# Performance work log

Measured on AMD Instinct MI355X. Metric: run time of the kernel, lower is better.

## Reference

```python
import jax, jax.numpy as jnp
import numpy as np


def _chamfer_single_directional(x, y):
    """Mean over batch of mean over points of min_j ||x_i - y_j||^2.

    x: [B, N, 3] (predicted), y: [B, M, 3] (target).
    Matches pytorch3d chamfer_distance(x, y, single_directional=True)
    with norm=2, point_reduction='mean', batch_reduction='mean'.
    """
    x2 = jnp.sum(x * x, axis=-1)                      # [B, N]
    y2 = jnp.sum(y * y, axis=-1)                      # [B, M]
    cross = jnp.einsum('bnd,bmd->bnm', x, y)          # [B, N, M]
    d2 = x2[:, :, None] + y2[:, None, :] - 2.0 * cross  # squared L2
    min_d2 = jnp.min(d2, axis=2)                      # [B, N] nearest in y
    return jnp.mean(jnp.mean(min_d2, axis=1))         # scalar


def setup_inputs() -> dict:
    key = jax.random.key(0)
    k1, k2 = jax.random.split(key)
    v = jax.random.normal(k1, (4, 8192, 3), dtype=jnp.float32)
    v_pred = jax.random.normal(k2, (4, 8192, 3), dtype=jnp.float32)
    return {"v": v, "v_pred": v_pred}


def reference(v, v_pred):
    # forward: chamfer_distance(v_pred, v, single_directional=True)
    return _chamfer_single_directional(v_pred, v)
```

## Files before the change

### kernel.cpp

```cpp
#include <hip/hip_runtime.h>

#define BB 4
#define NN 8192
#define MM 8192
#define BN (BB * NN)

#define BLK 256
#define QB  256
#define TC  1024
#define S   (MM / TC)
#define NJT (TC / 32)
#define NGRP ((NN / QB) * BB)

#define RB 32
#define GPB (NGRP / RB)

typedef __bf16 bf16x8 __attribute__((ext_vector_type(8)));
typedef float  f32x16 __attribute__((ext_vector_type(16)));


static __device__ inline void split_bf(float v, __bf16& h, __bf16& l) {
    h = (__bf16)v;
    l = (__bf16)(v - (float)h);
}

__global__ __launch_bounds__(BLK, 4) void chamfer_part(
    const float* __restrict__ y,
    const float* __restrict__ x,
    float* __restrict__ part)
{
    __shared__ uint4 FR[NJT * 64];
    __shared__ float red[QB];

    const int t   = threadIdx.x;
    const int l   = t & 63;
    const int w   = t >> 6;
    const int hi  = l >> 5;
    const int c32 = l & 31;
    const int ib  = blockIdx.x;
    const int s   = blockIdx.y;
    const int b   = blockIdx.z;
    const int g   = b * (NN / QB) + ib;

    {
        const float* xb = x + ((size_t)b * NN + (size_t)ib * QB) * 3;
        float x0 = xb[3*t+0], x1 = xb[3*t+1], x2 = xb[3*t+2];
        __bf16 h0,l0,h1,l1,h2,l2;
        split_bf(2.0f*x0, h0, l0);
        split_bf(2.0f*x1, h1, l1);
        split_bf(2.0f*x2, h2, l2);
        float nxx = -__builtin_fmaf(x2, x2, __builtin_fmaf(x1, x1, x0*x0));
        __bf16 hx, lx; split_bf(nxx, hx, lx);
        const __bf16 one = (__bf16)1.0f;
        bf16x8 g0 = {h0,h0,l0,l0,h1,h1,l1,l1};
        bf16x8 g1 = {h2,h2,l2,l2,hx,lx,one,one};
        const int at = t >> 5, col = t & 31;
        FR[at*64 +      col] = __builtin_bit_cast(uint4, g0);
        FR[at*64 + 32 + col] = __builtin_bit_cast(uint4, g1);
    }
    __syncthreads();
    const bf16x8 a0 = __builtin_bit_cast(bf16x8, FR[(w*2 + 0)*64 + l]);
    const bf16x8 a1 = __builtin_bit_cast(bf16x8, FR[(w*2 + 1)*64 + l]);
    __syncthreads();

    {
        const float* yb = y + ((size_t)b * MM + (size_t)s * TC) * 3;
        const __bf16 one = (__bf16)1.0f;
#pragma unroll
        for (int k2 = 0; k2 < 4; ++k2) {
            const int j = t + k2 * BLK;
            float y0 = yb[3*j+0], y1 = yb[3*j+1], y2 = yb[3*j+2];
            __bf16 h0,l0,h1,l1,h2,l2;
            split_bf(y0, h0, l0);
            split_bf(y1, h1, l1);
            split_bf(y2, h2, l2);
            float nyy = -__builtin_fmaf(y2, y2, __builtin_fmaf(y1, y1, y0*y0));
            __bf16 hy, ly; split_bf(nyy, hy, ly);
            bf16x8 g0 = {h0,l0,h0,l0,h1,l1,h1,l1};
            bf16x8 g1 = {h2,l2,h2,l2,one,one,hy,ly};
            const int jt = j >> 5, col = j & 31;
            FR[jt*64 +      col] = __builtin_bit_cast(uint4, g0);
            FR[jt*64 + 32 + col] = __builtin_bit_cast(uint4, g1);
        }
    }
    __syncthreads();

    f32x16 z;
#pragma unroll
    for (int r = 0; r < 16; ++r) z[r] = 0.0f;
    f32x16 best0, best1;
#pragma unroll
    for (int r = 0; r < 16; ++r) { best0[r] = -3.4e38f; best1[r] = -3.4e38f; }

#pragma unroll 1
    for (int jt = 0; jt < NJT; jt += 2) {
        const bf16x8 bf0 = __builtin_bit_cast(bf16x8, FR[jt*64 + l]);
        const bf16x8 bf1 = __builtin_bit_cast(bf16x8, FR[jt*64 + 64 + l]);
        f32x16 p = __builtin_amdgcn_mfma_f32_32x32x16_bf16(a0, bf0, z, 0, 0, 0);
        f32x16 q = __builtin_amdgcn_mfma_f32_32x32x16_bf16(a0, bf1, z, 0, 0, 0);
#pragma unroll
        for (int r = 0; r < 16; ++r)
            best0[r] = fmaxf(fmaxf(best0[r], p[r]), q[r]);
        p = __builtin_amdgcn_mfma_f32_32x32x16_bf16(a1, bf0, z, 0, 0, 0);
        q = __builtin_amdgcn_mfma_f32_32x32x16_bf16(a1, bf1, z, 0, 0, 0);
#pragma unroll
        for (int r = 0; r < 16; ++r)
            best1[r] = fmaxf(fmaxf(best1[r], p[r]), q[r]);
    }

#pragma unroll
    for (int ii = 0; ii < 2; ++ii) {
        const f32x16 bb = ii ? best1 : best0;
#pragma unroll
        for (int r = 0; r < 16; ++r) {
            float v = bb[r];
            v = fmaxf(v, __shfl_xor(v, 1, 64));
            v = fmaxf(v, __shfl_xor(v, 2, 64));
            v = fmaxf(v, __shfl_xor(v, 4, 64));
            v = fmaxf(v, __shfl_xor(v, 8, 64));
            v = fmaxf(v, __shfl_xor(v, 16, 64));
            if (c32 == 0) {
                const int qrow = (w*2 + ii)*32 + (r & 3) + 8*(r >> 2) + 4*hi;
                red[qrow] = -v;
            }
        }
    }
    __syncthreads();
    part[((size_t)g * S + s) * QB + t] = red[t];
}

__global__ __launch_bounds__(BLK) void reduce_groups(
    const float* __restrict__ part,
    float* __restrict__ ws2)
{
    const int t = threadIdx.x;
    float acc = 0.0f;
#pragma unroll
    for (int gi = 0; gi < GPB; ++gi) {
        const float* pg = part + ((size_t)(blockIdx.x * GPB + gi) * S) * QB;
        float dq = pg[t];
#pragma unroll
        for (int ss = 1; ss < S; ++ss)
            dq = fminf(dq, pg[ss * QB + t]);
        acc += dq;
    }
    for (int off = 32; off > 0; off >>= 1)
        acc += __shfl_down(acc, off, 64);
    __shared__ float wsum[4];
    if ((t & 63) == 0) wsum[t >> 6] = acc;
    __syncthreads();
    if (t == 0)
        ws2[blockIdx.x] = wsum[0] + wsum[1] + wsum[2] + wsum[3];
}

__global__ __launch_bounds__(64) void final32(
    const float* __restrict__ ws2,
    float* __restrict__ out)
{
    const int t = threadIdx.x;
    float v = (t < RB) ? ws2[t] : 0.0f;
    for (int off = 32; off > 0; off >>= 1)
        v += __shfl_down(v, off, 64);
    if (t == 0) out[0] = v * (1.0f / (float)BN);
}

extern "C" void kernel_launch(void* const* d_in, const int* in_sizes, int n_in,
                              void* d_out, int out_size, void* d_ws, size_t ws_size,
                              hipStream_t stream) {
    const float* v      = (const float*)d_in[0];
    const float* v_pred = (const float*)d_in[1];
    float* out = (float*)d_out;

    float* part = (float*)d_ws;
    float* ws2  = (float*)((char*)d_ws + (1u << 20));

    chamfer_part<<<dim3(NN / QB, S, BB), BLK, 0, stream>>>(v, v_pred, part);
    reduce_groups<<<RB, BLK, 0, stream>>>(part, ws2);
    final32<<<1, 64, 0, stream>>>(ws2, out);
}
```

Measured before the change: 73.44 us.

## Fuse chamfer over full target set with double-buffered LDS tiles, drop reduce kernel

```diff
diff --git a/kernel.cpp b/kernel.cpp
--- a/kernel.cpp
+++ b/kernel.cpp
@@ -5,15 +5,12 @@
 #define MM 8192
 #define BN (BB * NN)
 
-#define BLK 256
-#define QB  256
-#define TC  1024
-#define S   (MM / TC)
-#define NJT (TC / 32)
-#define NGRP ((NN / QB) * BB)
-
-#define RB 32
-#define GPB (NGRP / RB)
+#define QB   128
+#define BLK  512
+#define NCH  8
+#define TPC  1024
+#define NT   32
+#define NBLK ((NN / QB) * BB)
 
 typedef __bf16 bf16x8 __attribute__((ext_vector_type(8)));
 typedef float  f32x16 __attribute__((ext_vector_type(16)));
@@ -24,144 +21,154 @@
     l = (__bf16)(v - (float)h);
 }
 
-__global__ __launch_bounds__(BLK, 4) void chamfer_part(
+static __device__ inline void packB(float y0, float y1, float y2,
+                                    uint4& o0, uint4& o1) {
+    __bf16 h0,l0,h1,l1,h2,l2,hy,ly;
+    split_bf(y0, h0, l0);
+    split_bf(y1, h1, l1);
+    split_bf(y2, h2, l2);
+    float nyy = -__builtin_fmaf(y2, y2, __builtin_fmaf(y1, y1, y0*y0));
+    split_bf(nyy, hy, ly);
+    const __bf16 one = (__bf16)1.0f;
+    bf16x8 g0 = {h0,l0,h0,l0,h1,l1,h1,l1};
+    bf16x8 g1 = {h2,l2,h2,l2,one,one,hy,ly};
+    o0 = __builtin_bit_cast(uint4, g0);
+    o1 = __builtin_bit_cast(uint4, g1);
+}
+
+__global__ __launch_bounds__(BLK, 2) void chamfer_full(
     const float* __restrict__ y,
     const float* __restrict__ x,
-    float* __restrict__ part)
+    float* __restrict__ part1)
 {
-    __shared__ uint4 FR[NJT * 64];
-    __shared__ float red[QB];
+    __shared__ uint4 BIMG[2][NT * 64];
+    __shared__ uint4 AIMG[4 * 64];
+    __shared__ float red[2][QB];
+    __shared__ float ws8[8];
 
     const int t   = threadIdx.x;
     const int l   = t & 63;
     const int w   = t >> 6;
     const int hi  = l >> 5;
     const int c32 = l & 31;
-    const int ib  = blockIdx.x;
-    const int s   = blockIdx.y;
-    const int b   = blockIdx.z;
-    const int g   = b * (NN / QB) + ib;
+    const int at  = w >> 1;
+    const int jh  = w & 1;
 
-    {
-        const float* xb = x + ((size_t)b * NN + (size_t)ib * QB) * 3;
+    const float* yb = y + (size_t)blockIdx.y * MM * 3;
+
+    if (t < QB) {
+        const float* xb = x + ((size_t)blockIdx.y * NN
+                             + (size_t)blockIdx.x * QB) * 3;
         float x0 = xb[3*t+0], x1 = xb[3*t+1], x2 = xb[3*t+2];
-        __bf16 h0,l0,h1,l1,h2,l2;
+        __bf16 h0,l0,h1,l1,h2,l2,hx,lx;
         split_bf(2.0f*x0, h0, l0);
         split_bf(2.0f*x1, h1, l1);
         split_bf(2.0f*x2, h2, l2);
         float nxx = -__builtin_fmaf(x2, x2, __builtin_fmaf(x1, x1, x0*x0));
-        __bf16 hx, lx; split_bf(nxx, hx, lx);
+        split_bf(nxx, hx, lx);
         const __bf16 one = (__bf16)1.0f;
         bf16x8 g0 = {h0,h0,l0,l0,h1,h1,l1,l1};
         bf16x8 g1 = {h2,h2,l2,l2,hx,lx,one,one};
-        const int at = t >> 5, col = t & 31;
-        FR[at*64 +      col] = __builtin_bit_cast(uint4, g0);
-        FR[at*64 + 32 + col] = __builtin_bit_cast(uint4, g1);
+        AIMG[(t>>5)*64 +      (t&31)] = __builtin_bit_cast(uint4, g0);
+        AIMG[(t>>5)*64 + 32 + (t&31)] = __builtin_bit_cast(uint4, g1);
+    }
+    {
+        float u0 = yb[3*t+0],       u1 = yb[3*t+1],       u2 = yb[3*t+2];
+        float v0 = yb[3*(t+512)+0], v1 = yb[3*(t+512)+1], v2 = yb[3*(t+512)+2];
+        uint4 o0,o1,o2,o3;
+        packB(u0,u1,u2, o0,o1);
+        packB(v0,v1,v2, o2,o3);
+        BIMG[0][(t>>5)*64 +      (t&31)]       = o0;
+        BIMG[0][(t>>5)*64 + 32 + (t&31)]       = o1;
+        BIMG[0][((t+512)>>5)*64 +      (t&31)] = o2;
+        BIMG[0][((t+512)>>5)*64 + 32 + (t&31)] = o3;
     }
     __syncthreads();
-    const bf16x8 a0 = __builtin_bit_cast(bf16x8, FR[(w*2 + 0)*64 + l]);
-    const bf16x8 a1 = __builtin_bit_cast(bf16x8, FR[(w*2 + 1)*64 + l]);
-    __syncthreads();
-
-    {
-        const float* yb = y + ((size_t)b * MM + (size_t)s * TC) * 3;
-        const __bf16 one = (__bf16)1.0f;
-#pragma unroll
-        for (int k2 = 0; k2 < 4; ++k2) {
-            const int j = t + k2 * BLK;
-            float y0 = yb[3*j+0], y1 = yb[3*j+1], y2 = yb[3*j+2];
-            __bf16 h0,l0,h1,l1,h2,l2;
-            split_bf(y0, h0, l0);
-            split_bf(y1, h1, l1);
-            split_bf(y2, h2, l2);
-            float nyy = -__builtin_fmaf(y2, y2, __builtin_fmaf(y1, y1, y0*y0));
-            __bf16 hy, ly; split_bf(nyy, hy, ly);
-            bf16x8 g0 = {h0,l0,h0,l0,h1,l1,h1,l1};
-            bf16x8 g1 = {h2,l2,h2,l2,one,one,hy,ly};
-            const int jt = j >> 5, col = j & 31;
-            FR[jt*64 +      col] = __builtin_bit_cast(uint4, g0);
-            FR[jt*64 + 32 + col] = __builtin_bit_cast(uint4, g1);
-        }
-    }
-    __syncthreads();
+    const bf16x8 a0 = __builtin_bit_cast(bf16x8, AIMG[at*64 + hi*32 + c32]);
 
     f32x16 z;
 #pragma unroll
     for (int r = 0; r < 16; ++r) z[r] = 0.0f;
-    f32x16 best0, best1;
+    f32x16 best;
 #pragma unroll
-    for (int r = 0; r < 16; ++r) { best0[r] = -3.4e38f; best1[r] = -3.4e38f; }
+    for (int r = 0; r < 16; ++r) best[r] = -3.4e38f;
 
+    int cur = 0;
 #pragma unroll 1
-    for (int jt = 0; jt < NJT; jt += 2) {
-        const bf16x8 bf0 = __builtin_bit_cast(bf16x8, FR[jt*64 + l]);
-        const bf16x8 bf1 = __builtin_bit_cast(bf16x8, FR[jt*64 + 64 + l]);
-        f32x16 p = __builtin_amdgcn_mfma_f32_32x32x16_bf16(a0, bf0, z, 0, 0, 0);
-        f32x16 q = __builtin_amdgcn_mfma_f32_32x32x16_bf16(a0, bf1, z, 0, 0, 0);
+    for (int c = 0; c < NCH; ++c) {
+        float s0=0,s1=0,s2=0,s3=0,s4=0,s5=0;
+        const bool more = (c + 1 < NCH);
+        if (more) {
+            const float* yn = yb + (size_t)(c+1) * TPC * 3;
+            s0 = yn[3*t+0];       s1 = yn[3*t+1];       s2 = yn[3*t+2];
+            s3 = yn[3*(t+512)+0]; s4 = yn[3*(t+512)+1]; s5 = yn[3*(t+512)+2];
+        }
+        const uint4* B = BIMG[cur];
+        const int jb = jh * 16;
 #pragma unroll
-        for (int r = 0; r < 16; ++r)
-            best0[r] = fmaxf(fmaxf(best0[r], p[r]), q[r]);
-        p = __builtin_amdgcn_mfma_f32_32x32x16_bf16(a1, bf0, z, 0, 0, 0);
-        q = __builtin_amdgcn_mfma_f32_32x32x16_bf16(a1, bf1, z, 0, 0, 0);
+        for (int p2 = 0; p2 < 8; ++p2) {
+            bf16x8 c0 = __builtin_bit_cast(bf16x8, B[(jb + 2*p2    )*64 + l]);
+            bf16x8 c1 = __builtin_bit_cast(bf16x8, B[(jb + 2*p2 + 1)*64 + l]);
+            f32x16 p = __builtin_amdgcn_mfma_f32_32x32x16_bf16(a0, c0, z, 0, 0, 0);
+            f32x16 q = __builtin_amdgcn_mfma_f32_32x32x16_bf16(a0, c1, z, 0, 0, 0);
 #pragma unroll
-        for (int r = 0; r < 16; ++r)
-            best1[r] = fmaxf(fmaxf(best1[r], p[r]), q[r]);
+            for (int r = 0; r < 16; ++r)
+                best[r] = fmaxf(fmaxf(best[r], p[r]), q[r]);
+        }
+        if (more) {
+            uint4 o0,o1,o2,o3;
+            packB(s0,s1,s2, o0,o1);
+            packB(s3,s4,s5, o2,o3);
+            uint4* Bn = BIMG[cur ^ 1];
+            Bn[(t>>5)*64 +      (t&31)]       = o0;
+            Bn[(t>>5)*64 + 32 + (t&31)]       = o1;
+            Bn[((t+512)>>5)*64 +      (t&31)] = o2;
+            Bn[((t+512)>>5)*64 + 32 + (t&31)] = o3;
+            __syncthreads();
+            cur ^= 1;
+        }
     }
 
 #pragma unroll
-    for (int ii = 0; ii < 2; ++ii) {
-        const f32x16 bb = ii ? best1 : best0;
-#pragma unroll
-        for (int r = 0; r < 16; ++r) {
-            float v = bb[r];
-            v = fmaxf(v, __shfl_xor(v, 1, 64));
-            v = fmaxf(v, __shfl_xor(v, 2, 64));
-            v = fmaxf(v, __shfl_xor(v, 4, 64));
-            v = fmaxf(v, __shfl_xor(v, 8, 64));
-            v = fmaxf(v, __shfl_xor(v, 16, 64));
-            if (c32 == 0) {
-                const int qrow = (w*2 + ii)*32 + (r & 3) + 8*(r >> 2) + 4*hi;
-                red[qrow] = -v;
-            }
+    for (int r = 0; r < 16; ++r) {
+        float v = best[r];
+        v = fmaxf(v, __shfl_xor(v, 1, 64));
+        v = fmaxf(v, __shfl_xor(v, 2, 64));
+        v = fmaxf(v, __shfl_xor(v, 4, 64));
+        v = fmaxf(v, __shfl_xor(v, 8, 64));
+        v = fmaxf(v, __shfl_xor(v, 16, 64));
+        if (c32 == 0) {
+            const int row = (r & 3) + 8 * (r >> 2) + 4 * hi;
+            red[jh][at * 32 + row] = -v;
         }
     }
     __syncthreads();
-    part[((size_t)g * S + s) * QB + t] = red[t];
+    float m = (t < QB) ? fminf(red[0][t], red[1][t]) : 0.0f;
+    for (int off = 32; off > 0; off >>= 1)
+        m += __shfl_down(m, off, 64);
+    if (l == 0) ws8[w] = m;
+    __syncthreads();
+    if (t == 0) {
+        float s = 0.0f;
+#pragma unroll
+        for (int i = 0; i < 8; ++i) s += ws8[i];
+        part1[blockIdx.y * (NN / QB) + blockIdx.x] = s;
+    }
 }
 
-__global__ __launch_bounds__(BLK) void reduce_groups(
-    const float* __restrict__ part,
-    float* __restrict__ ws2)
-{
-    const int t = threadIdx.x;
-    float acc = 0.0f;
-#pragma unroll
-    for (int gi = 0; gi < GPB; ++gi) {
-        const float* pg = part + ((size_t)(blockIdx.x * GPB + gi) * S) * QB;
-        float dq = pg[t];
-#pragma unroll
-        for (int ss = 1; ss < S; ++ss)
-            dq = fminf(dq, pg[ss * QB + t]);
-        acc += dq;
-    }
-    for (int off = 32; off > 0; off >>= 1)
-        acc += __shfl_down(acc, off, 64);
-    __shared__ float wsum[4];
-    if ((t & 63) == 0) wsum[t >> 6] = acc;
-    __syncthreads();
-    if (t == 0)
-        ws2[blockIdx.x] = wsum[0] + wsum[1] + wsum[2] + wsum[3];
-}
-
-__global__ __launch_bounds__(64) void final32(
-    const float* __restrict__ ws2,
+__global__ __launch_bounds__(256) void final_sum256(
+    const float* __restrict__ part1,
     float* __restrict__ out)
 {
     const int t = threadIdx.x;
-    float v = (t < RB) ? ws2[t] : 0.0f;
+    float v = part1[t];
     for (int off = 32; off > 0; off >>= 1)
         v += __shfl_down(v, off, 64);
-    if (t == 0) out[0] = v * (1.0f / (float)BN);
+    __shared__ float ws[4];
+    if ((t & 63) == 0) ws[t >> 6] = v;
+    __syncthreads();
+    if (t == 0)
+        out[0] = (ws[0] + ws[1] + ws[2] + ws[3]) * (1.0f / (float)BN);
 }
 
 extern "C" void kernel_launch(void* const* d_in, const int* in_sizes, int n_in,
@@ -171,10 +178,8 @@
     const float* v_pred = (const float*)d_in[1];
     float* out = (float*)d_out;
 
-    float* part = (float*)d_ws;
-    float* ws2  = (float*)((char*)d_ws + (1u << 20));
+    float* part1 = (float*)d_ws;
 
-    chamfer_part<<<dim3(NN / QB, S, BB), BLK, 0, stream>>>(v, v_pred, part);
-    reduce_groups<<<RB, BLK, 0, stream>>>(part, ws2);
-    final32<<<1, 64, 0, stream>>>(ws2, out);
+    chamfer_full<<<dim3(NN / QB, BB), BLK, 0, stream>>>(v, v_pred, part1);
+    final_sum256<<<1, 256, 0, stream>>>(part1, out);
 }
```

Measured after the change: 131.5 us. 79.1% more time.
